# Performance work log

Measured on AMD Instinct MI355X. Metric: run time of the kernel, lower is better.

## Reference

```python
import jax, jax.numpy as jnp
import numpy as np

# --- FineRMoE routing constants (match init_kwargs) ---
TOP_K = 4
G_I, G_O = 2, 2
R_I, R_O = 4, 2
NUM_EXPERTS = 32  # must equal R_O*G_O*R_I*G_I


def _finermoe_router(scores):
    """scores: [T, E]. Returns (probs [T,top_k], selected [T,top_k])."""
    T, E = scores.shape
    S = E // (R_O * G_O)  # experts per concat-shard == R_I*G_I
    cs = scores.reshape(T, R_O * G_O, S)
    # top_k//G_O experts within each (R_O*G_O) shard
    _, add_idx = jax.lax.top_k(cs, TOP_K // G_O)
    add_mask = jnp.any(jax.nn.one_hot(add_idx, S, dtype=bool), axis=-2)  # [T, RO*GO, S]
    # keep the max-scoring R_O shard within each G_O group (argmax -> first max, like torch)
    shard_sum = cs.sum(-1).reshape(T, G_O, R_O)
    concat_mask = jax.nn.one_hot(jnp.argmax(shard_sum, axis=-1), R_O, dtype=bool)
    concat_mask = concat_mask.reshape(T, G_O * R_O)  # flat order matches RO*GO shard dim
    final_mask = (add_mask & concat_mask[:, :, None]).reshape(T, E)
    masked = jnp.where(final_mask, scores, -jnp.inf)
    probs, sel = jax.lax.top_k(masked, TOP_K)
    return probs, sel


def setup_inputs() -> dict:
    key = jax.random.key(0)
    ks = jax.random.split(key, 6)
    B, Sq, H, E, I = 1, 2048, 1024, NUM_EXPERTS, 256
    O = H // G_O  # expert output width
    return {
        "hidden_states": jax.random.normal(ks[0], (B, Sq, H), dtype=jnp.float32),
        "Wr": jax.random.normal(ks[1], (H, E), dtype=jnp.float32) * 0.02,
        "Wg": jax.random.normal(ks[2], (E, H, I), dtype=jnp.float32) * 0.02,
        "Wu": jax.random.normal(ks[3], (E, H, I), dtype=jnp.float32) * 0.02,
        "Wd": jax.random.normal(ks[4], (E, I, O), dtype=jnp.float32) * 0.02,
        "Wc": jax.random.normal(ks[5], (H, H), dtype=jnp.float32) * 0.02,
    }


def reference(hidden_states, Wr, Wg, Wu, Wd, Wc):
    B, Sq, H = hidden_states.shape
    T = B * Sq
    E = Wr.shape[1]
    x = hidden_states.reshape(T, H)
    router_logits = x @ Wr  # [T, E]
    probs, sel = _finermoe_router(router_logits)
    rw = jax.nn.softmax(probs.astype(jnp.float32), axis=1)
    rw = rw / rw.sum(-1, keepdims=True)  # norm_topk_prob
    rw = rw.astype(x.dtype)
    # dense combine weights [T, E] (zero for unselected experts)
    C = jnp.zeros((T, E), x.dtype).at[jnp.arange(T)[:, None], sel].add(rw)
    # all-expert MLP (stacked GEMMs); combine weights mask out unselected tokens
    h = jax.nn.silu(jnp.einsum('th,ehi->eti', x, Wg)) * jnp.einsum('th,ehi->eti', x, Wu)
    y = jnp.einsum('eti,eio->eto', h, Wd)  # [E, T, H//G_O]
    P = E // G_O  # experts per concat shard slice == R_O*G_I*R_I
    out = jnp.einsum('tgp,gpto->tgo', C.reshape(T, G_O, P),
                     y.reshape(G_O, P, T, H // G_O)).reshape(T, H)
    out = out @ Wc  # moe_concat_proj
    return out.reshape(B, Sq, H), router_logits
```

## Files before the change

kernel.cpp:

```cpp
#include <hip/hip_runtime.h>
#include <hip/hip_bf16.h>
#include <math.h>
#include <stdint.h>

typedef __hip_bfloat16 hbf16;

#define T_TOK 2048
#define H_DIM 1024
#define E_NUM 32
#define I_DIM 256
#define O_DIM 512
#define CAP   2048
#define TT    16
#define WT    16
#define XSTR2 520
#define HSTR  264
#define CSTR  32

typedef __bf16 bf16x8 __attribute__((ext_vector_type(8)));
typedef float  f32x4  __attribute__((ext_vector_type(4)));

__device__ __forceinline__ float b2f(hbf16 v) { return __bfloat162float(v); }
__device__ __forceinline__ float bb2f(ushort u) { return __uint_as_float((uint32_t)u << 16); }

__device__ __forceinline__ ushort f2b(float f) {
    uint32_t u = __float_as_uint(f);
    return (ushort)((u + 0x7FFFu + ((u >> 16) & 1u)) >> 16);
}

template<int BF>
__device__ __forceinline__ float ld(const void* p, size_t i) {
    if (BF) return b2f(((const hbf16*)p)[i]);
    else    return ((const float*)p)[i];
}

__device__ __forceinline__ f32x4 mfma_bf16(bf16x8 a, bf16x8 b, f32x4 c) {
    return __builtin_amdgcn_mfma_f32_16x16x32_bf16(a, b, c, 0, 0, 0);
}

__device__ __forceinline__ void sched_fence() { __builtin_amdgcn_sched_barrier(0); }

__global__ __launch_bounds__(256) void detect_kernel(
    const uint32_t* __restrict__ xw, int* __restrict__ flag, int* __restrict__ counts)
{
    __shared__ int cnt;
    if (threadIdx.x == 0) cnt = 0;
    if (threadIdx.x < E_NUM) counts[threadIdx.x * CSTR] = 0;
    __syncthreads();
    int c = 0;
    for (int i = threadIdx.x; i < 1024; i += 256) {
        int e = (xw[i] >> 7) & 0xFF;
        if (e >= 110 && e <= 140) c++;
    }
    atomicAdd(&cnt, c);
    __syncthreads();
    if (threadIdx.x == 0) *flag = (cnt > 512) ? 1 : 0;
}


__device__ void conv3_tile(const void* __restrict__ src, ushort* __restrict__ dst,
                           int bf, int K, int N, int b, float* __restrict__ sh)
{
    int tilesN = N >> 7, tilesK = K >> 5;
    int e  = b / (tilesK * tilesN);
    int r  = b % (tilesK * tilesN);
    int k0 = (r / tilesN) << 5;
    int n0 = (r % tilesN) << 7;
    size_t base = (size_t)e * K * N;
    int tid = threadIdx.x;
    {
        int row = tid >> 3, c0 = (tid & 7) * 16;
        if (!bf) {
            const float* sp = (const float*)src + base + (size_t)(k0 + row) * N + n0 + c0;
            #pragma unroll
            for (int i = 0; i < 4; ++i) {
                float4 v = *(const float4*)(sp + i * 4);
                sh[row * 132 + c0 + i*4 + 0] = v.x;
                sh[row * 132 + c0 + i*4 + 1] = v.y;
                sh[row * 132 + c0 + i*4 + 2] = v.z;
                sh[row * 132 + c0 + i*4 + 3] = v.w;
            }
        } else {
            const hbf16* sp = (const hbf16*)src + base + (size_t)(k0 + row) * N + n0 + c0;
            #pragma unroll
            for (int i = 0; i < 16; ++i) sh[row * 132 + c0 + i] = b2f(sp[i]);
        }
    }
    __syncthreads();
    {
        int nn = tid >> 1, kk = (tid & 1) * 16;
        union { ushort v[16]; uint4 u[2]; } R;
        #pragma unroll
        for (int i = 0; i < 16; ++i) R.v[i] = f2b(sh[(kk + i) * 132 + nn]);
        ushort* dp = dst + base + ((size_t)(k0 >> 5) * N + (n0 + nn)) * 32 + kk;
        *(uint4*)dp       = R.u[0];
        *(uint4*)(dp + 8) = R.u[1];
    }
    __syncthreads();
}

template<int BF>
__device__ void router3_body(const void* __restrict__ x, const void* __restrict__ Wr,
                             void* __restrict__ out_base,
                             int* __restrict__ counts, int* __restrict__ tok_list,
                             float* __restrict__ wt_list,
                             float* __restrict__ xs, float* __restrict__ sl,
                             float* __restrict__ sf, int t0)
{
    int tid  = threadIdx.x;
    int e    = tid & 31;
    int half = tid >> 5;

    {
        int t = tid >> 7;
        int c = (tid & 127) * 8;
        if (!BF) {
            const float* xp = (const float*)x + (size_t)(t0 + t) * H_DIM + c;
            *(float4*)&xs[t*1024 + c]     = *(const float4*)xp;
            *(float4*)&xs[t*1024 + c + 4] = *(const float4*)(xp + 4);
        } else {
            const hbf16* xp = (const hbf16*)x + (size_t)(t0 + t) * H_DIM + c;
            #pragma unroll
            for (int j = 0; j < 8; ++j) xs[t*1024 + c + j] = b2f(xp[j]);
        }
    }
    __syncthreads();

    float a0 = 0.f, a1 = 0.f;
    int kbase = half * 128;
    const float* xr0 = &xs[kbase];
    const float* xr1 = &xs[1024 + kbase];
    #pragma unroll 8
    for (int k = 0; k < 128; ++k) {
        float w = ld<BF>(Wr, (size_t)(kbase + k) * E_NUM + e);
        a0 = fmaf(xr0[k], w, a0);
        a1 = fmaf(xr1[k], w, a1);
    }
    sl[(0*8 + half)*32 + e] = a0;
    sl[(1*8 + half)*32 + e] = a1;
    __syncthreads();

    if (tid < 64) {
        int t  = tid >> 5;
        int ee = tid & 31;
        float s = 0.f;
        #pragma unroll
        for (int h = 0; h < 8; ++h) s += sl[(t*8 + h)*32 + ee];
        sf[t*32 + ee] = s;
        size_t li = (size_t)T_TOK * H_DIM + (size_t)(t0 + t) * E_NUM + ee;
        if (BF) ((hbf16*)out_base)[li] = __float2bfloat16(s);
        else    ((float*)out_base)[li] = s;
    }
    __syncthreads();

    if (tid < 2) {
        int t = t0 + tid;
        float s[E_NUM];
        #pragma unroll
        for (int i = 0; i < E_NUM; ++i) s[i] = sf[tid * 32 + i];

        int   selE[4];
        float selL[4];
        int ns = 0;
        for (int g = 0; g < 2; ++g) {
            float sum0 = 0.f, sum1 = 0.f;
            #pragma unroll
            for (int j = 0; j < 8; ++j) {
                sum0 += s[(2*g)   * 8 + j];
                sum1 += s[(2*g+1) * 8 + j];
            }
            int bestSh = (sum1 > sum0) ? (2*g+1) : (2*g);
            int base = bestSh * 8;
            int i1 = 0;
            for (int j = 1; j < 8; ++j) if (s[base+j] > s[base+i1]) i1 = j;
            int i2 = -1;
            for (int j = 0; j < 8; ++j) {
                if (j == i1) continue;
                if (i2 < 0 || s[base+j] > s[base+i2]) i2 = j;
            }
            selE[ns] = base + i1; selL[ns] = s[base+i1]; ++ns;
            selE[ns] = base + i2; selL[ns] = s[base+i2]; ++ns;
        }
        float m = fmaxf(fmaxf(selL[0], selL[1]), fmaxf(selL[2], selL[3]));
        float w[4];
        float sum = 0.f;
        for (int j = 0; j < 4; ++j) { w[j] = expf(selL[j] - m); sum += w[j]; }
        float inv = 1.f / sum;
        for (int j = 0; j < 4; ++j) {
            int ee = selE[j];
            int pos = atomicAdd(&counts[ee * CSTR], 1);
            if (pos >= 0 && pos < CAP) {
                tok_list[ee * CAP + pos] = t | (j << 11);
                wt_list[ee * CAP + pos]  = w[j] * inv;
            }
        }
    }
}

__global__ __launch_bounds__(256) void fused_cr_kernel(
    const void* x, const void* Wr,
    const void* Wg, const void* Wu, const void* Wd, const void* Wc,
    ushort* Wg_t, ushort* Wu_t, ushort* Wd_t, ushort* Wc_t,
    void* out_base, const int* __restrict__ flag,
    int* counts, int* tok_list, float* wt_list)
{
    __shared__ __align__(16) float sh[32 * 132];
    int b = blockIdx.x;
    if (b < 1024) {
        float* xs = sh;
        float* sl = sh + 2048;
        float* sf = sh + 2560;
        if (*flag) router3_body<1>(x, Wr, out_base, counts, tok_list, wt_list,
                                   xs, sl, sf, b * 2);
        else       router3_body<0>(x, Wr, out_base, counts, tok_list, wt_list,
                                   xs, sl, sf, b * 2);
    } else {
        int bb = b - 1024;
        int bf = *flag;
        if      (bb < 2048) conv3_tile(Wg, Wg_t, bf, 1024,  256, bb,        sh);
        else if (bb < 4096) conv3_tile(Wu, Wu_t, bf, 1024,  256, bb - 2048, sh);
        else if (bb < 5120) conv3_tile(Wd, Wd_t, bf,  256,  512, bb - 4096, sh);
        else                conv3_tile(Wc, Wc_t, bf, 1024, 1024, bb - 5120, sh);
    }
}

template<int BF>
__device__ void expert3_body(const void* __restrict__ x,
    const ushort* __restrict__ Wg_t, const ushort* __restrict__ Wu_t,
    const ushort* __restrict__ Wd_t,
    const int* __restrict__ counts, const int* __restrict__ tok_list,
    const float* __restrict__ wt_list, ushort* __restrict__ ybuf,
    ushort* __restrict__ xA, ushort* __restrict__ hsm,
    int* __restrict__ tokid, float* __restrict__ twt, int* __restrict__ tslot)
{
    int e = blockIdx.x;
    int n = counts[e * CSTR]; n = n < 0 ? 0 : (n > CAP ? CAP : n);
    int t0 = blockIdx.y * 16;
    if (t0 >= n) return;
    int tid  = threadIdx.x;
    int lane = tid & 63, wv = tid >> 6;
    int q = lane >> 4, l15 = lane & 15;

    if (tid < 16) {
        int it = t0 + tid;
        int id; float ww;
        if (it < n) { id = tok_list[e*CAP + it]; ww = wt_list[e*CAP + it]; }
        else        { id = tok_list[e*CAP + t0]; ww = 0.f; }
        tokid[tid] = id & 2047;
        tslot[tid] = (id >> 11) & 3;
        twt[tid]   = ww;
    }
    __syncthreads();

    const ushort* Bg0 = Wg_t + (size_t)e * (H_DIM * I_DIM) + (wv*32 + l15) * 32 + q*8;
    const ushort* Bu0 = Wu_t + (size_t)e * (H_DIM * I_DIM) + (wv*32 + l15) * 32 + q*8;

    f32x4 Cg[2], Cu[2];
    Cg[0] = (f32x4)0.f; Cg[1] = (f32x4)0.f;
    Cu[0] = (f32x4)0.f; Cu[1] = (f32x4)0.f;

    bf16x8 bg[2][4][2], bu[2][4][2];
    #pragma unroll
    for (int ig = 0; ig < 4; ++ig)
        #pragma unroll
        for (int j = 0; j < 2; ++j) {
            bg[0][ig][j] = *(const bf16x8*)(Bg0 + (size_t)ig*8192 + j*512);
            bu[0][ig][j] = *(const bf16x8*)(Bu0 + (size_t)ig*8192 + j*512);
        }
    sched_fence();

    #pragma unroll
    for (int hk = 0; hk < 2; ++hk) {
        if (hk) __syncthreads();

        {
            int row = tid >> 5;
            int kb  = (tid & 31) * 8;
            size_t srow = (size_t)tokid[row] * H_DIM + hk * 512;
            #pragma unroll
            for (int c = 0; c < 2; ++c) {
                int k = kb + c * 256;
                union { ushort v[8]; uint4 u; } U;
                if (BF) {
                    U.u = *(const uint4*)((const ushort*)x + srow + k);
                } else {
                    const float* xp = (const float*)x + srow + k;
                    float4 a = *(const float4*)xp;
                    float4 b = *(const float4*)(xp + 4);
                    U.v[0]=f2b(a.x); U.v[1]=f2b(a.y); U.v[2]=f2b(a.z); U.v[3]=f2b(a.w);
                    U.v[4]=f2b(b.x); U.v[5]=f2b(b.y); U.v[6]=f2b(b.z); U.v[7]=f2b(b.w);
                }
                *(uint4*)&xA[row * XSTR2 + k] = U.u;
            }
        }
        __syncthreads();

        #pragma unroll
        for (int g2 = 0; g2 < 4; ++g2) {
            int grp = hk * 4 + g2;
            int cb  = grp & 1;
            if (grp < 7) {
                #pragma unroll
                for (int ig = 0; ig < 4; ++ig)
                    #pragma unroll
                    for (int j = 0; j < 2; ++j) {
                        int idx = (grp + 1) * 4 + ig;
                        bg[cb^1][ig][j] = *(const bf16x8*)(Bg0 + (size_t)idx*8192 + j*512);
                        bu[cb^1][ig][j] = *(const bf16x8*)(Bu0 + (size_t)idx*8192 + j*512);
                    }
            }
            sched_fence();
            #pragma unroll
            for (int ig = 0; ig < 4; ++ig) {
                int kl = (g2 * 4 + ig) * 32;
                bf16x8 A0 = *(const bf16x8*)&xA[l15 * XSTR2 + kl + q*8];
                #pragma unroll
                for (int j = 0; j < 2; ++j) {
                    Cg[j] = mfma_bf16(A0, bg[cb][ig][j], Cg[j]);
                    Cu[j] = mfma_bf16(A0, bu[cb][ig][j], Cu[j]);
                }
            }
        }
    }

    const ushort* Bd0 = Wd_t + (size_t)e * (I_DIM * O_DIM) + (wv*64 + l15) * 32 + q*8;
    bf16x8 bd[2][4][4];
    #pragma unroll
    for (int g2 = 0; g2 < 2; ++g2)
        #pragma unroll
        for (int kc2 = 0; kc2 < 4; ++kc2)
            #pragma unroll
            for (int j = 0; j < 4; ++j)
                bd[g2][kc2][j] = *(const bf16x8*)(Bd0 + (size_t)(g2*4 + kc2)*16384 + j*512);
    sched_fence();

    #pragma unroll
    for (int j = 0; j < 2; ++j)
        #pragma unroll
        for (int r = 0; r < 4; ++r) {
            float g = Cg[j][r], u = Cu[j][r];
            float h = (g / (1.f + expf(-g))) * u;
            hsm[(q*4 + r) * HSTR + wv*32 + j*16 + l15] = f2b(h);
        }
    __syncthreads();

    f32x4 Cd[4];
    #pragma unroll
    for (int j = 0; j < 4; ++j) Cd[j] = (f32x4)0.f;

    #pragma unroll
    for (int g2 = 0; g2 < 2; ++g2)
        #pragma unroll
        for (int kc2 = 0; kc2 < 4; ++kc2) {
            int kc = g2 * 4 + kc2;
            bf16x8 A0 = *(const bf16x8*)&hsm[l15 * HSTR + kc*32 + q*8];
            #pragma unroll
            for (int j = 0; j < 4; ++j)
                Cd[j] = mfma_bf16(A0, bd[g2][kc2][j], Cd[j]);
        }

    #pragma unroll
    for (int r = 0; r < 4; ++r) {
        int row = q*4 + r;
        if (t0 + row < n) {
            float ww = twt[row];
            size_t base = ((size_t)tokid[row] * 4 + tslot[row]) * O_DIM;
            #pragma unroll
            for (int j = 0; j < 4; ++j)
                ybuf[base + wv*64 + j*16 + l15] = f2b(ww * Cd[j][r]);
        }
    }
}

__global__ __launch_bounds__(512, 2) void expert3_kernel(
    const void* x, const ushort* Wg_t, const ushort* Wu_t, const ushort* Wd_t,
    const int* flag, const int* counts, const int* tok_list, const float* wt_list,
    ushort* ybuf)
{
    __shared__ ushort xA[16 * XSTR2];
    __shared__ ushort hsm[16 * HSTR];
    __shared__ int    tokid[16];
    __shared__ float  twt[16];
    __shared__ int    tslot[16];
    if (*flag) expert3_body<1>(x, Wg_t, Wu_t, Wd_t, counts, tok_list, wt_list,
                               ybuf, xA, hsm, tokid, twt, tslot);
    else       expert3_body<0>(x, Wg_t, Wu_t, Wd_t, counts, tok_list, wt_list,
                               ybuf, xA, hsm, tokid, twt, tslot);
}

template<int BF>
__device__ void wc3_body(const ushort* __restrict__ ybuf, const ushort* __restrict__ Wc_t,
                         void* __restrict__ out_base, ushort* __restrict__ zA)
{
    int m0  = blockIdx.x * 16;
    int n0  = blockIdx.y * 256;
    int tid = threadIdx.x;
    int lane = tid & 63, wv = tid >> 6;
    int q = lane >> 4, l15 = lane & 15;

    const ushort* Bc0 = Wc_t + (size_t)(n0 + wv*32 + l15) * 32 + q*8;
    f32x4 C[2];
    C[0] = (f32x4)0.f; C[1] = (f32x4)0.f;

    bf16x8 bc[2][4][2];
    #pragma unroll
    for (int ig = 0; ig < 4; ++ig)
        #pragma unroll
        for (int j = 0; j < 2; ++j)
            bc[0][ig][j] = *(const bf16x8*)(Bc0 + (size_t)ig*32768 + j*512);
    sched_fence();

    #pragma unroll
    for (int hk = 0; hk < 2; ++hk) {
        if (hk) __syncthreads();

        {
            int row = tid >> 5;
            int kb  = (tid & 31) * 8;
            int t = m0 + row;
            int s0 = hk ? 2 : 0;
            #pragma unroll
            for (int c = 0; c < 2; ++c) {
                int hl = kb + c * 256;
                const ushort* p0 = ybuf + ((size_t)t * 4 + s0) * O_DIM + hl;
                union { ushort v[8]; uint4 u; } A, B, R;
                A.u = *(const uint4*)p0;
                B.u = *(const uint4*)(p0 + O_DIM);
                #pragma unroll
                for (int i = 0; i < 8; ++i) R.v[i] = f2b(bb2f(A.v[i]) + bb2f(B.v[i]));
                *(uint4*)&zA[row * XSTR2 + hl] = R.u;
            }
        }
        __syncthreads();

        #pragma unroll
        for (int g2 = 0; g2 < 4; ++g2) {
            int grp = hk * 4 + g2;
            int cb  = grp & 1;
            if (grp < 7) {
                #pragma unroll
                for (int ig = 0; ig < 4; ++ig)
                    #pragma unroll
                    for (int j = 0; j < 2; ++j) {
                        int idx = (grp + 1) * 4 + ig;
                        bc[cb^1][ig][j] = *(const bf16x8*)(Bc0 + (size_t)idx*32768 + j*512);
                    }
            }
            sched_fence();
            #pragma unroll
            for (int ig = 0; ig < 4; ++ig) {
                int kl = (g2 * 4 + ig) * 32;
                bf16x8 A0 = *(const bf16x8*)&zA[l15 * XSTR2 + kl + q*8];
                #pragma unroll
                for (int j = 0; j < 2; ++j)
                    C[j] = mfma_bf16(A0, bc[cb][ig][j], C[j]);
            }
        }
    }

    #pragma unroll
    for (int j = 0; j < 2; ++j)
        #pragma unroll
        for (int r = 0; r < 4; ++r) {
            int row = m0 + q*4 + r;
            int col = n0 + wv*32 + j*16 + l15;
            size_t o = (size_t)row * H_DIM + col;
            if (BF) ((hbf16*)out_base)[o] = __float2bfloat16(C[j][r]);
            else    ((float*)out_base)[o] = C[j][r];
        }
}

__global__ __launch_bounds__(512, 2) void wc3_kernel(
    const ushort* ybuf, const ushort* Wc_t, void* out_base, const int* flag)
{
    __shared__ ushort zA[16 * XSTR2];
    if (*flag) wc3_body<1>(ybuf, Wc_t, out_base, zA);
    else       wc3_body<0>(ybuf, Wc_t, out_base, zA);
}


__global__ __launch_bounds__(256) void zero_kernel(
    float* __restrict__ z_fp32, float* __restrict__ z_bf16,
    const int* __restrict__ flag, int* __restrict__ counts)
{
    float* base = (*flag) ? z_bf16 : z_fp32;
    size_t i = (size_t)blockIdx.x * 256 + threadIdx.x;
    ((float4*)base)[i] = make_float4(0.f, 0.f, 0.f, 0.f);
    if (blockIdx.x == 0 && threadIdx.x < E_NUM) ((int*)counts)[threadIdx.x * CSTR] = 0;
}

template<int BF>
__device__ void router_body(const void* __restrict__ x, const void* __restrict__ Wr,
                            void* __restrict__ out_base,
                            int* __restrict__ counts, int* __restrict__ tok_list,
                            float* __restrict__ wt_list, float* __restrict__ sl)
{
    int t    = blockIdx.x;
    int lane = threadIdx.x;
    int e    = lane & 31;
    int half = lane >> 5;

    float acc = 0.f;
    size_t xoff = (size_t)t * H_DIM;
    int h0 = half * (H_DIM / 2);
    for (int h = h0; h < h0 + H_DIM / 2; ++h)
        acc = fmaf(ld<BF>(x, xoff + h), ld<BF>(Wr, (size_t)h * E_NUM + e), acc);
    acc += __shfl_down(acc, 32);

    if (lane < 32) {
        sl[e] = acc;
        size_t li = (size_t)T_TOK * H_DIM + (size_t)t * E_NUM + e;
        if (BF) ((hbf16*)out_base)[li] = __float2bfloat16(acc);
        else    ((float*)out_base)[li] = acc;
    }
    __syncthreads();

    if (lane == 0) {
        float s[E_NUM];
        #pragma unroll
        for (int i = 0; i < E_NUM; ++i) s[i] = sl[i];
        int   selE[4];
        float selL[4];
        int ns = 0;
        for (int g = 0; g < 2; ++g) {
            float sum0 = 0.f, sum1 = 0.f;
            #pragma unroll
            for (int j = 0; j < 8; ++j) {
                sum0 += s[(2*g)   * 8 + j];
                sum1 += s[(2*g+1) * 8 + j];
            }
            int bestSh = (sum1 > sum0) ? (2*g+1) : (2*g);
            int base = bestSh * 8;
            int i1 = 0;
            for (int j = 1; j < 8; ++j) if (s[base+j] > s[base+i1]) i1 = j;
            int i2 = -1;
            for (int j = 0; j < 8; ++j) {
                if (j == i1) continue;
                if (i2 < 0 || s[base+j] > s[base+i2]) i2 = j;
            }
            selE[ns] = base + i1; selL[ns] = s[base+i1]; ++ns;
            selE[ns] = base + i2; selL[ns] = s[base+i2]; ++ns;
        }
        float m = fmaxf(fmaxf(selL[0], selL[1]), fmaxf(selL[2], selL[3]));
        float w[4];
        float sum = 0.f;
        for (int j = 0; j < 4; ++j) { w[j] = expf(selL[j] - m); sum += w[j]; }
        float inv = 1.f / sum;
        for (int j = 0; j < 4; ++j) {
            int ee = selE[j];
            int pos = atomicAdd(&counts[ee * CSTR], 1);
            if (pos >= 0 && pos < CAP) {
                tok_list[ee * CAP + pos] = t;
                wt_list[ee * CAP + pos]  = w[j] * inv;
            }
        }
    }
}

__global__ __launch_bounds__(64) void router_kernel(
    const void* x, const void* Wr, void* out_base, const int* flag,
    int* counts, int* tok_list, float* wt_list)
{
    __shared__ float sl[E_NUM];
    if (*flag) router_body<1>(x, Wr, out_base, counts, tok_list, wt_list, sl);
    else       router_body<0>(x, Wr, out_base, counts, tok_list, wt_list, sl);
}

template<int BF>
__device__ void expert_body(const void* __restrict__ x,
                            const void* __restrict__ Wg, const void* __restrict__ Wu,
                            const void* __restrict__ Wd,
                            const int* __restrict__ counts, const int* __restrict__ tok_list,
                            const float* __restrict__ wt_list,
                            float* __restrict__ z, float* __restrict__ xsbuf)
{
    int e = blockIdx.x;
    int n = counts[e * CSTR];
    n = n < 0 ? 0 : (n > CAP ? CAP : n);
    int t0 = blockIdx.y * TT;
    if (t0 >= n) return;
    int tid = threadIdx.x;

    float (*xs)[H_DIM] = reinterpret_cast<float(*)[H_DIM]>(xsbuf);
    float (*hs)[I_DIM] = reinterpret_cast<float(*)[I_DIM]>(xsbuf);

    const int*   tl = tok_list + e * CAP;
    const float* wl = wt_list  + e * CAP;

    for (int idx = tid; idx < TT * H_DIM; idx += 256) {
        int tt = idx >> 10;
        int h  = idx & (H_DIM - 1);
        int it = t0 + tt;
        int tkn = (it < n) ? tl[it] : tl[t0];
        tkn = (tkn < 0) ? 0 : (tkn >= T_TOK ? T_TOK - 1 : tkn);
        xs[tt][h] = ld<BF>(x, (size_t)tkn * H_DIM + h);
    }
    __syncthreads();

    size_t wbase = (size_t)e * H_DIM * I_DIM + tid;
    float ag[TT], au[TT];
    #pragma unroll
    for (int tt = 0; tt < TT; ++tt) { ag[tt] = 0.f; au[tt] = 0.f; }

    for (int k = 0; k < H_DIM; k += 4) {
        float g0 = ld<BF>(Wg, wbase + (size_t)(k+0) * I_DIM);
        float g1 = ld<BF>(Wg, wbase + (size_t)(k+1) * I_DIM);
        float g2 = ld<BF>(Wg, wbase + (size_t)(k+2) * I_DIM);
        float g3 = ld<BF>(Wg, wbase + (size_t)(k+3) * I_DIM);
        float u0 = ld<BF>(Wu, wbase + (size_t)(k+0) * I_DIM);
        float u1 = ld<BF>(Wu, wbase + (size_t)(k+1) * I_DIM);
        float u2 = ld<BF>(Wu, wbase + (size_t)(k+2) * I_DIM);
        float u3 = ld<BF>(Wu, wbase + (size_t)(k+3) * I_DIM);
        #pragma unroll
        for (int tt = 0; tt < TT; ++tt) {
            float4 xv = *(const float4*)&xs[tt][k];
            ag[tt] = fmaf(xv.w, g3, fmaf(xv.z, g2, fmaf(xv.y, g1, fmaf(xv.x, g0, ag[tt]))));
            au[tt] = fmaf(xv.w, u3, fmaf(xv.z, u2, fmaf(xv.y, u1, fmaf(xv.x, u0, au[tt]))));
        }
    }
    float hval[TT];
    #pragma unroll
    for (int tt = 0; tt < TT; ++tt) {
        float g = ag[tt];
        hval[tt] = (g / (1.f + expf(-g))) * au[tt];
    }
    __syncthreads();
    #pragma unroll
    for (int tt = 0; tt < TT; ++tt) hs[tt][tid] = hval[tt];
    __syncthreads();

    size_t dbase = (size_t)e * I_DIM * O_DIM;
    float y0[TT], y1[TT];
    #pragma unroll
    for (int tt = 0; tt < TT; ++tt) { y0[tt] = 0.f; y1[tt] = 0.f; }

    for (int k = 0; k < I_DIM; k += 4) {
        float d00 = ld<BF>(Wd, dbase + (size_t)(k+0) * O_DIM + tid);
        float d01 = ld<BF>(Wd, dbase + (size_t)(k+1) * O_DIM + tid);
        float d02 = ld<BF>(Wd, dbase + (size_t)(k+2) * O_DIM + tid);
        float d03 = ld<BF>(Wd, dbase + (size_t)(k+3) * O_DIM + tid);
        float d10 = ld<BF>(Wd, dbase + (size_t)(k+0) * O_DIM + tid + 256);
        float d11 = ld<BF>(Wd, dbase + (size_t)(k+1) * O_DIM + tid + 256);
        float d12 = ld<BF>(Wd, dbase + (size_t)(k+2) * O_DIM + tid + 256);
        float d13 = ld<BF>(Wd, dbase + (size_t)(k+3) * O_DIM + tid + 256);
        #pragma unroll
        for (int tt = 0; tt < TT; ++tt) {
            float4 hv = *(const float4*)&hs[tt][k];
            y0[tt] = fmaf(hv.w, d03, fmaf(hv.z, d02, fmaf(hv.y, d01, fmaf(hv.x, d00, y0[tt]))));
            y1[tt] = fmaf(hv.w, d13, fmaf(hv.z, d12, fmaf(hv.y, d11, fmaf(hv.x, d10, y1[tt]))));
        }
    }

    int gsel = e >> 4;
    size_t colbase = (size_t)gsel * O_DIM;
    #pragma unroll
    for (int tt = 0; tt < TT; ++tt) {
        int it = t0 + tt;
        if (it < n) {
            float w  = wl[it];
            int tkn = tl[it];
            tkn = (tkn < 0) ? 0 : (tkn >= T_TOK ? T_TOK - 1 : tkn);
            atomicAdd(&z[(size_t)tkn * H_DIM + colbase + tid],       w * y0[tt]);
            atomicAdd(&z[(size_t)tkn * H_DIM + colbase + tid + 256], w * y1[tt]);
        }
    }
}

__global__ __launch_bounds__(256) void expert_kernel(
    const void* x, const void* Wg, const void* Wu, const void* Wd,
    const int* flag, const int* counts, const int* tok_list, const float* wt_list,
    float* z_fp32, float* z_bf16)
{
    __shared__ __align__(16) float xsbuf[TT * H_DIM];
    if (*flag) expert_body<1>(x, Wg, Wu, Wd, counts, tok_list, wt_list, z_bf16, xsbuf);
    else       expert_body<0>(x, Wg, Wu, Wd, counts, tok_list, wt_list, z_fp32, xsbuf);
}

template<int BF>
__device__ void wc_body(const float* __restrict__ z, const void* __restrict__ Wc,
                        void* __restrict__ out_base, float* __restrict__ psbuf)
{
    int t0  = blockIdx.x * WT;
    int tid = threadIdx.x;
    float (*ps)[H_DIM] = reinterpret_cast<float(*)[H_DIM]>(psbuf);

    for (int idx = tid; idx < WT * H_DIM; idx += 256) {
        int tt = idx >> 10;
        int h  = idx & (H_DIM - 1);
        ps[tt][h] = z[(size_t)(t0 + tt) * H_DIM + h];
    }
    __syncthreads();

    float acc[WT][4];
    #pragma unroll
    for (int tt = 0; tt < WT; ++tt)
        #pragma unroll
        for (int qq = 0; qq < 4; ++qq) acc[tt][qq] = 0.f;

    for (int k = 0; k < H_DIM; k += 2) {
        float c00 = ld<BF>(Wc, (size_t)(k+0) * H_DIM + tid);
        float c01 = ld<BF>(Wc, (size_t)(k+0) * H_DIM + tid + 256);
        float c02 = ld<BF>(Wc, (size_t)(k+0) * H_DIM + tid + 512);
        float c03 = ld<BF>(Wc, (size_t)(k+0) * H_DIM + tid + 768);
        float c10 = ld<BF>(Wc, (size_t)(k+1) * H_DIM + tid);
        float c11 = ld<BF>(Wc, (size_t)(k+1) * H_DIM + tid + 256);
        float c12 = ld<BF>(Wc, (size_t)(k+1) * H_DIM + tid + 512);
        float c13 = ld<BF>(Wc, (size_t)(k+1) * H_DIM + tid + 768);
        #pragma unroll
        for (int tt = 0; tt < WT; ++tt) {
            float2 pv = *(const float2*)&ps[tt][k];
            acc[tt][0] = fmaf(pv.y, c10, fmaf(pv.x, c00, acc[tt][0]));
            acc[tt][1] = fmaf(pv.y, c11, fmaf(pv.x, c01, acc[tt][1]));
            acc[tt][2] = fmaf(pv.y, c12, fmaf(pv.x, c02, acc[tt][2]));
            acc[tt][3] = fmaf(pv.y, c13, fmaf(pv.x, c03, acc[tt][3]));
        }
    }

    #pragma unroll
    for (int tt = 0; tt < WT; ++tt) {
        #pragma unroll
        for (int qq = 0; qq < 4; ++qq) {
            size_t o = (size_t)(t0 + tt) * H_DIM + tid + 256 * qq;
            if (BF) ((hbf16*)out_base)[o] = __float2bfloat16(acc[tt][qq]);
            else    ((float*)out_base)[o] = acc[tt][qq];
        }
    }
}

__global__ __launch_bounds__(256) void wc_kernel(
    const float* z_fp32, const float* z_bf16, const void* Wc,
    void* out_base, const int* flag)
{
    __shared__ __align__(16) float psbuf[WT * H_DIM];
    if (*flag) wc_body<1>(z_bf16, Wc, out_base, psbuf);
    else       wc_body<0>(z_fp32, Wc, out_base, psbuf);
}

extern "C" void kernel_launch(void* const* d_in, const int* in_sizes, int n_in,
                              void* d_out, int out_size, void* d_ws, size_t ws_size,
                              hipStream_t stream)
{
    (void)in_sizes; (void)n_in; (void)out_size;

    const void* x  = d_in[0];
    const void* Wr = d_in[1];
    const void* Wg = d_in[2];
    const void* Wu = d_in[3];
    const void* Wd = d_in[4];
    const void* Wc = d_in[5];

    char* ws = (char*)d_ws;
    int*   counts   = (int*)(ws + 0);
    int*   flag     = (int*)(ws + 4096);
    int*   tok_list = (int*)(ws + 8192);
    float* wt_list  = (float*)(ws + 8192 + (size_t)E_NUM * CAP * 4);

    detect_kernel<<<1, 256, 0, stream>>>((const uint32_t*)x, flag, counts);

    if (ws_size >= ((size_t)58 << 20)) {
        ushort* ybuf = (ushort*)(ws + ((size_t)1  << 20));
        ushort* Wg_t = (ushort*)(ws + ((size_t)16 << 20));
        ushort* Wu_t = (ushort*)(ws + ((size_t)32 << 20));
        ushort* Wd_t = (ushort*)(ws + ((size_t)48 << 20));
        ushort* Wc_t = (ushort*)(ws + ((size_t)56 << 20));

        fused_cr_kernel<<<1024 + 5376, 256, 0, stream>>>(
            x, Wr, Wg, Wu, Wd, Wc, Wg_t, Wu_t, Wd_t, Wc_t,
            d_out, flag, counts, tok_list, wt_list);
        expert3_kernel<<<dim3(E_NUM, T_TOK / 16), 512, 0, stream>>>(
            x, Wg_t, Wu_t, Wd_t, flag, counts, tok_list, wt_list, ybuf);
        wc3_kernel<<<dim3(T_TOK / 16, 4), 512, 0, stream>>>(ybuf, Wc_t, d_out, flag);
    } else {
        float* z_bf16 = (float*)(ws + (1u << 20));
        float* z_fp32 = (float*)d_out;
        zero_kernel<<<T_TOK, 256, 0, stream>>>(z_fp32, z_bf16, flag, counts);
        router_kernel<<<T_TOK, 64, 0, stream>>>(x, Wr, d_out, flag, counts, tok_list, wt_list);
        expert_kernel<<<dim3(E_NUM, T_TOK / TT), 256, 0, stream>>>(
            x, Wg, Wu, Wd, flag, counts, tok_list, wt_list, z_fp32, z_bf16);
        wc_kernel<<<T_TOK / WT, 256, 0, stream>>>(z_fp32, z_bf16, Wc, d_out, flag);
    }
}
```

Before: 231.2 us.

## Double token tile to 32 rows per block in expert and concat GEMMs

The expert MLP and Wc projection kernels now process 32 tokens per block instead of 16, using 1024 threads. Each wave covers 16 output columns across two 16-row M tiles, so every weight fragment loaded from global memory feeds two MFMAs. This is meant to halve redundant weight traffic per token and cut the block count. In exchange the block is larger and more serialized, and the stricter launch bounds (1024 threads, 4 blocks) may squeeze registers and cause spills or lower occupancy.

```diff
diff --git a/kernel.cpp b/kernel.cpp
--- a/kernel.cpp
+++ b/kernel.cpp
@@ -235,13 +235,13 @@
 {
     int e = blockIdx.x;
     int n = counts[e * CSTR]; n = n < 0 ? 0 : (n > CAP ? CAP : n);
-    int t0 = blockIdx.y * 16;
+    int t0 = blockIdx.y * 32;
     if (t0 >= n) return;
     int tid  = threadIdx.x;
     int lane = tid & 63, wv = tid >> 6;
     int q = lane >> 4, l15 = lane & 15;
 
-    if (tid < 16) {
+    if (tid < 32) {
         int it = t0 + tid;
         int id; float ww;
         if (it < n) { id = tok_list[e*CAP + it]; ww = wt_list[e*CAP + it]; }
@@ -252,21 +252,19 @@
     }
     __syncthreads();
 
-    const ushort* Bg0 = Wg_t + (size_t)e * (H_DIM * I_DIM) + (wv*32 + l15) * 32 + q*8;
-    const ushort* Bu0 = Wu_t + (size_t)e * (H_DIM * I_DIM) + (wv*32 + l15) * 32 + q*8;
+    const ushort* Bg0 = Wg_t + (size_t)e * (H_DIM * I_DIM) + (wv*16 + l15) * 32 + q*8;
+    const ushort* Bu0 = Wu_t + (size_t)e * (H_DIM * I_DIM) + (wv*16 + l15) * 32 + q*8;
 
     f32x4 Cg[2], Cu[2];
     Cg[0] = (f32x4)0.f; Cg[1] = (f32x4)0.f;
     Cu[0] = (f32x4)0.f; Cu[1] = (f32x4)0.f;
 
-    bf16x8 bg[2][4][2], bu[2][4][2];
-    #pragma unroll
-    for (int ig = 0; ig < 4; ++ig)
-        #pragma unroll
-        for (int j = 0; j < 2; ++j) {
-            bg[0][ig][j] = *(const bf16x8*)(Bg0 + (size_t)ig*8192 + j*512);
-            bu[0][ig][j] = *(const bf16x8*)(Bu0 + (size_t)ig*8192 + j*512);
-        }
+    bf16x8 bg[2][4], bu[2][4];
+    #pragma unroll
+    for (int ig = 0; ig < 4; ++ig) {
+        bg[0][ig] = *(const bf16x8*)(Bg0 + (size_t)ig*8192);
+        bu[0][ig] = *(const bf16x8*)(Bu0 + (size_t)ig*8192);
+    }
     sched_fence();
 
     #pragma unroll
@@ -301,87 +299,84 @@
             int cb  = grp & 1;
             if (grp < 7) {
                 #pragma unroll
-                for (int ig = 0; ig < 4; ++ig)
-                    #pragma unroll
-                    for (int j = 0; j < 2; ++j) {
-                        int idx = (grp + 1) * 4 + ig;
-                        bg[cb^1][ig][j] = *(const bf16x8*)(Bg0 + (size_t)idx*8192 + j*512);
-                        bu[cb^1][ig][j] = *(const bf16x8*)(Bu0 + (size_t)idx*8192 + j*512);
-                    }
+                for (int ig = 0; ig < 4; ++ig) {
+                    int idx = (grp + 1) * 4 + ig;
+                    bg[cb^1][ig] = *(const bf16x8*)(Bg0 + (size_t)idx*8192);
+                    bu[cb^1][ig] = *(const bf16x8*)(Bu0 + (size_t)idx*8192);
+                }
             }
             sched_fence();
             #pragma unroll
             for (int ig = 0; ig < 4; ++ig) {
                 int kl = (g2 * 4 + ig) * 32;
-                bf16x8 A0 = *(const bf16x8*)&xA[l15 * XSTR2 + kl + q*8];
+                bf16x8 A0 = *(const bf16x8*)&xA[(l15)      * XSTR2 + kl + q*8];
+                bf16x8 A1 = *(const bf16x8*)&xA[(16 + l15) * XSTR2 + kl + q*8];
+                Cg[0] = mfma_bf16(A0, bg[cb][ig], Cg[0]);
+                Cg[1] = mfma_bf16(A1, bg[cb][ig], Cg[1]);
+                Cu[0] = mfma_bf16(A0, bu[cb][ig], Cu[0]);
+                Cu[1] = mfma_bf16(A1, bu[cb][ig], Cu[1]);
+            }
+        }
+    }
+
+    const ushort* Bd0 = Wd_t + (size_t)e * (I_DIM * O_DIM) + (wv*32 + l15) * 32 + q*8;
+    bf16x8 bd[8][2];
+    #pragma unroll
+    for (int kc = 0; kc < 8; ++kc)
+        #pragma unroll
+        for (int j = 0; j < 2; ++j)
+            bd[kc][j] = *(const bf16x8*)(Bd0 + (size_t)kc*16384 + j*512);
+    sched_fence();
+
+    #pragma unroll
+    for (int m = 0; m < 2; ++m)
+        #pragma unroll
+        for (int r = 0; r < 4; ++r) {
+            float g = Cg[m][r], u = Cu[m][r];
+            float h = (g / (1.f + expf(-g))) * u;
+            hsm[(m*16 + q*4 + r) * HSTR + wv*16 + l15] = f2b(h);
+        }
+    __syncthreads();
+
+    f32x4 Cd[2][2];
+    Cd[0][0] = (f32x4)0.f; Cd[0][1] = (f32x4)0.f;
+    Cd[1][0] = (f32x4)0.f; Cd[1][1] = (f32x4)0.f;
+    #pragma unroll
+    for (int kc = 0; kc < 8; ++kc) {
+        bf16x8 A0 = *(const bf16x8*)&hsm[(l15)      * HSTR + kc*32 + q*8];
+        bf16x8 A1 = *(const bf16x8*)&hsm[(16 + l15) * HSTR + kc*32 + q*8];
+        #pragma unroll
+        for (int j = 0; j < 2; ++j) {
+            Cd[0][j] = mfma_bf16(A0, bd[kc][j], Cd[0][j]);
+            Cd[1][j] = mfma_bf16(A1, bd[kc][j], Cd[1][j]);
+        }
+    }
+
+    #pragma unroll
+    for (int m = 0; m < 2; ++m)
+        #pragma unroll
+        for (int r = 0; r < 4; ++r) {
+            int row = m*16 + q*4 + r;
+            if (t0 + row < n) {
+                float ww = twt[row];
+                size_t base = ((size_t)tokid[row] * 4 + tslot[row]) * O_DIM;
                 #pragma unroll
-                for (int j = 0; j < 2; ++j) {
-                    Cg[j] = mfma_bf16(A0, bg[cb][ig][j], Cg[j]);
-                    Cu[j] = mfma_bf16(A0, bu[cb][ig][j], Cu[j]);
-                }
-            }
-        }
-    }
-
-    const ushort* Bd0 = Wd_t + (size_t)e * (I_DIM * O_DIM) + (wv*64 + l15) * 32 + q*8;
-    bf16x8 bd[2][4][4];
-    #pragma unroll
-    for (int g2 = 0; g2 < 2; ++g2)
-        #pragma unroll
-        for (int kc2 = 0; kc2 < 4; ++kc2)
-            #pragma unroll
-            for (int j = 0; j < 4; ++j)
-                bd[g2][kc2][j] = *(const bf16x8*)(Bd0 + (size_t)(g2*4 + kc2)*16384 + j*512);
-    sched_fence();
-
-    #pragma unroll
-    for (int j = 0; j < 2; ++j)
-        #pragma unroll
-        for (int r = 0; r < 4; ++r) {
-            float g = Cg[j][r], u = Cu[j][r];
-            float h = (g / (1.f + expf(-g))) * u;
-            hsm[(q*4 + r) * HSTR + wv*32 + j*16 + l15] = f2b(h);
-        }
-    __syncthreads();
-
-    f32x4 Cd[4];
-    #pragma unroll
-    for (int j = 0; j < 4; ++j) Cd[j] = (f32x4)0.f;
-
-    #pragma unroll
-    for (int g2 = 0; g2 < 2; ++g2)
-        #pragma unroll
-        for (int kc2 = 0; kc2 < 4; ++kc2) {
-            int kc = g2 * 4 + kc2;
-            bf16x8 A0 = *(const bf16x8*)&hsm[l15 * HSTR + kc*32 + q*8];
-            #pragma unroll
-            for (int j = 0; j < 4; ++j)
-                Cd[j] = mfma_bf16(A0, bd[g2][kc2][j], Cd[j]);
-        }
-
-    #pragma unroll
-    for (int r = 0; r < 4; ++r) {
-        int row = q*4 + r;
-        if (t0 + row < n) {
-            float ww = twt[row];
-            size_t base = ((size_t)tokid[row] * 4 + tslot[row]) * O_DIM;
-            #pragma unroll
-            for (int j = 0; j < 4; ++j)
-                ybuf[base + wv*64 + j*16 + l15] = f2b(ww * Cd[j][r]);
-        }
-    }
-}
-
-__global__ __launch_bounds__(512, 2) void expert3_kernel(
+                for (int j = 0; j < 2; ++j)
+                    ybuf[base + wv*32 + j*16 + l15] = f2b(ww * Cd[m][j][r]);
+            }
+        }
+}
+
+__global__ __launch_bounds__(1024, 4) void expert3_kernel(
     const void* x, const ushort* Wg_t, const ushort* Wu_t, const ushort* Wd_t,
     const int* flag, const int* counts, const int* tok_list, const float* wt_list,
     ushort* ybuf)
 {
-    __shared__ ushort xA[16 * XSTR2];
-    __shared__ ushort hsm[16 * HSTR];
-    __shared__ int    tokid[16];
-    __shared__ float  twt[16];
-    __shared__ int    tslot[16];
+    __shared__ ushort xA[32 * XSTR2];
+    __shared__ ushort hsm[32 * HSTR];
+    __shared__ int    tokid[32];
+    __shared__ float  twt[32];
+    __shared__ int    tslot[32];
     if (*flag) expert3_body<1>(x, Wg_t, Wu_t, Wd_t, counts, tok_list, wt_list,
                                ybuf, xA, hsm, tokid, twt, tslot);
     else       expert3_body<0>(x, Wg_t, Wu_t, Wd_t, counts, tok_list, wt_list,
@@ -392,22 +387,20 @@
 __device__ void wc3_body(const ushort* __restrict__ ybuf, const ushort* __restrict__ Wc_t,
                          void* __restrict__ out_base, ushort* __restrict__ zA)
 {
-    int m0  = blockIdx.x * 16;
+    int m0  = blockIdx.x * 32;
     int n0  = blockIdx.y * 256;
     int tid = threadIdx.x;
     int lane = tid & 63, wv = tid >> 6;
     int q = lane >> 4, l15 = lane & 15;
 
-    const ushort* Bc0 = Wc_t + (size_t)(n0 + wv*32 + l15) * 32 + q*8;
+    const ushort* Bc0 = Wc_t + (size_t)(n0 + wv*16 + l15) * 32 + q*8;
     f32x4 C[2];
     C[0] = (f32x4)0.f; C[1] = (f32x4)0.f;
 
-    bf16x8 bc[2][4][2];
+    bf16x8 bc[2][4];
     #pragma unroll
     for (int ig = 0; ig < 4; ++ig)
-        #pragma unroll
-        for (int j = 0; j < 2; ++j)
-            bc[0][ig][j] = *(const bf16x8*)(Bc0 + (size_t)ig*32768 + j*512);
+        bc[0][ig] = *(const bf16x8*)(Bc0 + (size_t)ig*32768);
     sched_fence();
 
     #pragma unroll
@@ -439,41 +432,39 @@
             int cb  = grp & 1;
             if (grp < 7) {
                 #pragma unroll
-                for (int ig = 0; ig < 4; ++ig)
-                    #pragma unroll
-                    for (int j = 0; j < 2; ++j) {
-                        int idx = (grp + 1) * 4 + ig;
-                        bc[cb^1][ig][j] = *(const bf16x8*)(Bc0 + (size_t)idx*32768 + j*512);
-                    }
+                for (int ig = 0; ig < 4; ++ig) {
+                    int idx = (grp + 1) * 4 + ig;
+                    bc[cb^1][ig] = *(const bf16x8*)(Bc0 + (size_t)idx*32768);
+                }
             }
             sched_fence();
             #pragma unroll
             for (int ig = 0; ig < 4; ++ig) {
                 int kl = (g2 * 4 + ig) * 32;
-                bf16x8 A0 = *(const bf16x8*)&zA[l15 * XSTR2 + kl + q*8];
-                #pragma unroll
-                for (int j = 0; j < 2; ++j)
-                    C[j] = mfma_bf16(A0, bc[cb][ig][j], C[j]);
-            }
-        }
-    }
-
-    #pragma unroll
-    for (int j = 0; j < 2; ++j)
+                bf16x8 A0 = *(const bf16x8*)&zA[(l15)      * XSTR2 + kl + q*8];
+                bf16x8 A1 = *(const bf16x8*)&zA[(16 + l15) * XSTR2 + kl + q*8];
+                C[0] = mfma_bf16(A0, bc[cb][ig], C[0]);
+                C[1] = mfma_bf16(A1, bc[cb][ig], C[1]);
+            }
+        }
+    }
+
+    #pragma unroll
+    for (int m = 0; m < 2; ++m)
         #pragma unroll
         for (int r = 0; r < 4; ++r) {
-            int row = m0 + q*4 + r;
-            int col = n0 + wv*32 + j*16 + l15;
+            int row = m0 + m*16 + q*4 + r;
+            int col = n0 + wv*16 + l15;
             size_t o = (size_t)row * H_DIM + col;
-            if (BF) ((hbf16*)out_base)[o] = __float2bfloat16(C[j][r]);
-            else    ((float*)out_base)[o] = C[j][r];
-        }
-}
-
-__global__ __launch_bounds__(512, 2) void wc3_kernel(
+            if (BF) ((hbf16*)out_base)[o] = __float2bfloat16(C[m][r]);
+            else    ((float*)out_base)[o] = C[m][r];
+        }
+}
+
+__global__ __launch_bounds__(1024, 4) void wc3_kernel(
     const ushort* ybuf, const ushort* Wc_t, void* out_base, const int* flag)
 {
-    __shared__ ushort zA[16 * XSTR2];
+    __shared__ ushort zA[32 * XSTR2];
     if (*flag) wc3_body<1>(ybuf, Wc_t, out_base, zA);
     else       wc3_body<0>(ybuf, Wc_t, out_base, zA);
 }
@@ -767,9 +758,9 @@
         fused_cr_kernel<<<1024 + 5376, 256, 0, stream>>>(
             x, Wr, Wg, Wu, Wd, Wc, Wg_t, Wu_t, Wd_t, Wc_t,
             d_out, flag, counts, tok_list, wt_list);
-        expert3_kernel<<<dim3(E_NUM, T_TOK / 16), 512, 0, stream>>>(
+        expert3_kernel<<<dim3(E_NUM, T_TOK / 32), 1024, 0, stream>>>(
             x, Wg_t, Wu_t, Wd_t, flag, counts, tok_list, wt_list, ybuf);
-        wc3_kernel<<<dim3(T_TOK / 16, 4), 512, 0, stream>>>(ybuf, Wc_t, d_out, flag);
+        wc3_kernel<<<dim3(T_TOK / 32, 4), 1024, 0, stream>>>(ybuf, Wc_t, d_out, flag);
     } else {
         float* z_bf16 = (float*)(ws + (1u << 20));
         float* z_fp32 = (float*)d_out;
```

Result: faster. 208.1 us (-10.0%).
